# Kernel tuning notes

Measured on AMD Instinct MI355X. Metric: run time of the kernel, lower is better.

The kernel has to match this reference:

```python
import jax, jax.numpy as jnp
import numpy as np

GROUP_SIZE = 64
IN_F, OUT_F, RANK = 4096, 4096, 32
N_TOKENS = 4096
N_GROUPS = IN_F // GROUP_SIZE


def setup_inputs() -> dict:
    key = jax.random.key(0)
    k = jax.random.split(key, 6)
    x = jax.random.normal(k[0], (N_TOKENS, IN_F), dtype=jnp.float32)
    # signed int4 values in [-8, 7], stored unpacked as int32
    main_qweight = jax.random.randint(k[1], (OUT_F, N_GROUPS, GROUP_SIZE), -8, 8, dtype=jnp.int32)
    main_wscale = jax.random.uniform(k[2], (OUT_F, N_GROUPS), dtype=jnp.float32) * 0.02 + 1e-3
    bias = jax.random.normal(k[3], (OUT_F,), dtype=jnp.float32) * 0.02
    proj_down_dense = jax.random.normal(k[4], (IN_F, RANK), dtype=jnp.float32) * 0.02
    proj_up_dense = jax.random.normal(k[5], (RANK, OUT_F), dtype=jnp.float32) * 0.02
    return {
        "x": x,
        "main_qweight": main_qweight,
        "main_wscale": main_wscale,
        "bias": bias,
        "proj_down_dense": proj_down_dense,
        "proj_up_dense": proj_up_dense,
    }


def reference(x, main_qweight, main_wscale, bias, proj_down_dense, proj_up_dense):
    n = x.shape[0]
    # --- per-group int8 activation quantization (symmetric, max-abs/127) ---
    xg = x.reshape(n, N_GROUPS, GROUP_SIZE).astype(jnp.float32)  # [N, G, gs]
    max_abs = jnp.max(jnp.abs(xg), axis=-1, keepdims=True)
    ascale = jnp.where(max_abs > 0, max_abs * (1.0 / 127.0), jnp.ones_like(max_abs))
    qx = jnp.clip(jnp.round(xg / ascale), -127.0, 127.0)
    # Fold per-group activation scales back in; per (out, group) weight scales into weight.
    # out[n,o] = sum_g ascale[n,g] * wscale[o,g] * sum_k qx[n,g,k] * qw[o,g,k]
    a_deq = (qx * ascale).reshape(n, IN_F)                                   # [N, in]
    w_deq = (main_qweight.astype(jnp.float32) * main_wscale[..., None]).reshape(OUT_F, IN_F)  # [out, in]
    out = a_deq @ w_deq.T + bias.astype(jnp.float32)                          # [N, out], fp32 accumulate
    # --- SVD low-rank correction: x @ proj_down @ proj_up (down in x dtype, up in fp32) ---
    low_rank = x @ proj_down_dense                                            # [N, rank]
    out = out + low_rank.astype(jnp.float32) @ proj_up_dense.astype(jnp.float32)
    return out.astype(x.dtype)
```

## Files before the change

kernel.cpp:

```cpp
#include <hip/hip_runtime.h>
#include <hip/hip_bf16.h>

#define IN_F  4096
#define OUT_F 4096
#define NTOK  4096
#define RANK  32
#define GS    64
#define NG    64
#define KTOT  4224
#define NKT   66
#define ITERS 33
#define KCH   1024

typedef __attribute__((ext_vector_type(4))) float f32x4;
typedef __attribute__((ext_vector_type(8))) short bf16x8;

__device__ __forceinline__ ushort f2bf(float f) {
  union { float f; uint u; } c; c.f = f;
  const uint u = c.u;
  return (ushort)((u + 0x7fffu + ((u >> 16) & 1u)) >> 16);
}

__global__ __launch_bounds__(256)
void quant_kernel(const float* __restrict__ x, ushort* __restrict__ Aext)
{
  const int tid  = threadIdx.x;
  const int wave = tid >> 6, lane = tid & 63;
  const int sub  = lane & 15;
  const int ggrp = blockIdx.x * 16 + wave * 4 + (lane >> 4);
  const int row  = ggrp >> 6, g = ggrp & 63;

  const float4 v = *(const float4*)(x + (size_t)row * IN_F + g * GS + sub * 4);
  float m = fmaxf(fmaxf(fabsf(v.x), fabsf(v.y)), fmaxf(fabsf(v.z), fabsf(v.w)));
  m = fmaxf(m, __shfl_xor(m, 1));
  m = fmaxf(m, __shfl_xor(m, 2));
  m = fmaxf(m, __shfl_xor(m, 4));
  m = fmaxf(m, __shfl_xor(m, 8));
  const float ascale = (m > 0.f) ? m * (1.f / 127.f) : 1.f;

  const float d0 = fminf(fmaxf(rintf(v.x / ascale), -127.f), 127.f) * ascale;
  const float d1 = fminf(fmaxf(rintf(v.y / ascale), -127.f), 127.f) * ascale;
  const float d2 = fminf(fmaxf(rintf(v.z / ascale), -127.f), 127.f) * ascale;
  const float d3 = fminf(fmaxf(rintf(v.w / ascale), -127.f), 127.f) * ascale;

  uint2 st;
  st.x = (uint)f2bf(d0) | ((uint)f2bf(d1) << 16);
  st.y = (uint)f2bf(d2) | ((uint)f2bf(d3) << 16);
  *(uint2*)(Aext + (size_t)row * KTOT + g * GS + sub * 4) = st;
}

__global__ __launch_bounds__(256)
void wdeq_kernel(const int* __restrict__ qw, const float* __restrict__ wsc,
                 ushort* __restrict__ Bext)
{
  const int gidx = blockIdx.x * 256 + threadIdx.x;
  const int o  = gidx >> 9;
  const int i0 = (gidx & 511) << 3;
  const float sc = wsc[o * NG + (i0 >> 6)];
  const int4 qa = *(const int4*)(qw + (size_t)o * IN_F + i0);
  const int4 qb = *(const int4*)(qw + (size_t)o * IN_F + i0 + 4);
  uint4 st;
  st.x = (uint)f2bf(qa.x * sc) | ((uint)f2bf(qa.y * sc) << 16);
  st.y = (uint)f2bf(qa.z * sc) | ((uint)f2bf(qa.w * sc) << 16);
  st.z = (uint)f2bf(qb.x * sc) | ((uint)f2bf(qb.y * sc) << 16);
  st.w = (uint)f2bf(qb.z * sc) | ((uint)f2bf(qb.w * sc) << 16);
  *(uint4*)(Bext + (size_t)o * KTOT + i0) = st;
}

__global__ __launch_bounds__(256)
void aux_kernel(const float* __restrict__ pd, const float* __restrict__ pu,
                ushort* __restrict__ Bext, ushort* __restrict__ pdT)
{
  const int id = blockIdx.x * 256 + threadIdx.x;
  ushort* dst = Bext + (size_t)id * KTOT + IN_F;
  #pragma unroll
  for (int r = 0; r < RANK; ++r) {
    dst[r]            = f2bf(pu[(size_t)r * OUT_F + id]);
    dst[RANK + r]     = 0;
    dst[2 * RANK + r] = 0;
    dst[3 * RANK + r] = 0;
  }
  #pragma unroll
  for (int r = 0; r < RANK; ++r)
    pdT[(size_t)r * IN_F + id] = f2bf(pd[(size_t)id * RANK + r]);
}

__global__ __launch_bounds__(256)
void lr_kernel(const ushort* __restrict__ A, const ushort* __restrict__ pdT,
               float* __restrict__ part)
{
  __shared__ alignas(16) ushort lA[64 * 64];
  const int tid  = threadIdx.x;
  const int wave = tid >> 6, lane = tid & 63;
  const int mt = blockIdx.x >> 2;
  const int kc = blockIdx.x & 3;
  const int k0 = kc * KCH;

  const int tr  = tid >> 3;
  const int scc = (tid & 7) ^ (tr & 7);
  const ushort* aSrc = A + (size_t)(mt * 64 + tr) * KTOT + k0 + scc * 8;
  char* ldsA = (char*)lA + wave * 1024;

  f32x4 acc[2];
  #pragma unroll
  for (int n = 0; n < 2; ++n) acc[n] = f32x4{0.f, 0.f, 0.f, 0.f};

  for (int kt = 0; kt < KCH / 64; ++kt) {
    const ushort* aS = aSrc + kt * 64;
    #pragma unroll
    for (int j = 0; j < 2; ++j)
      __builtin_amdgcn_global_load_lds(
          (const __attribute__((address_space(1))) void*)(aS + (size_t)j * 32 * KTOT),
          (__attribute__((address_space(3))) void*)(ldsA + j * 4096), 16, 0, 0);
    __syncthreads();
    #pragma unroll
    for (int ks = 0; ks < 2; ++ks) {
      const int kb  = (ks * 32 + (lane >> 4) * 8) * 2;
      const int row = wave * 16 + (lane & 15);
      const int addr = (row * 128 + kb) ^ ((row & 7) << 4);
      bf16x8 af = *(const bf16x8*)((const char*)lA + addr);
      #pragma unroll
      for (int n = 0; n < 2; ++n) {
        const int prow = n * 16 + (lane & 15);
        bf16x8 bf = *(const bf16x8*)(pdT + (size_t)prow * IN_F + k0 + kt * 64 + ks * 32 + (lane >> 4) * 8);
        acc[n] = __builtin_amdgcn_mfma_f32_16x16x32_bf16(af, bf, acc[n], 0, 0, 0);
      }
    }
    __syncthreads();
  }
  const int r0   = lane & 15;
  const int rowb = mt * 64 + wave * 16 + (lane >> 4) * 4;
  #pragma unroll
  for (int n = 0; n < 2; ++n)
    #pragma unroll
    for (int i = 0; i < 4; ++i)
      part[((size_t)kc * 4096 + rowb + i) * 32 + n * 16 + r0] = acc[n][i];
}

__global__ __launch_bounds__(256)
void lrcomb_kernel(const float* __restrict__ part, ushort* __restrict__ Aext)
{
  const int id  = blockIdx.x * 256 + threadIdx.x;
  const int row = id >> 5, r = id & 31;
  const float s = part[(size_t)row * 32 + r]
                + part[(size_t)(4096 + row) * 32 + r]
                + part[(size_t)(8192 + row) * 32 + r]
                + part[(size_t)(12288 + row) * 32 + r];
  ushort* dst = Aext + (size_t)row * KTOT + IN_F;
  dst[r]            = f2bf(s);
  dst[RANK + r]     = 0;
  dst[2 * RANK + r] = 0;
  dst[3 * RANK + r] = 0;
}

__device__ __forceinline__ void stageA(const ushort* __restrict__ Atile, char* lds,
                                       int b, int h, int kt, int w, int lane)
{
  #pragma unroll
  for (int l = 0; l < 2; ++l) {
    const int g = w * 2 + l;
    const int quarter = h + (g >> 3) * 2;
    const int sub = g & 7;
    const int grow = quarter * 64 + sub * 8 + (lane >> 3);
    const ushort* src = Atile + (size_t)grow * KTOT + kt * 64 + (((lane & 7) ^ (lane >> 3)) << 3);
    __builtin_amdgcn_global_load_lds(
        (const __attribute__((address_space(1))) void*)src,
        (__attribute__((address_space(3))) void*)(lds + b * 32768 + quarter * 8192 + sub * 1024),
        16, 0, 0);
  }
}

__device__ __forceinline__ void stageB(const ushort* __restrict__ Btile, char* lds,
                                       int b, int h, int kt, int w, int lane)
{
  #pragma unroll
  for (int l = 0; l < 2; ++l) {
    const int g = w * 2 + l;
    const int j = g >> 2;
    const int sub = g & 3;
    const int grow = j * 64 + h * 32 + sub * 8 + (lane >> 3);
    const ushort* src = Btile + (size_t)grow * KTOT + kt * 64 + (((lane & 7) ^ (lane >> 3)) << 3);
    __builtin_amdgcn_global_load_lds(
        (const __attribute__((address_space(1))) void*)src,
        (__attribute__((address_space(3))) void*)(lds + 65536 + b * 32768 + j * 8192 + h * 4096 + sub * 1024),
        16, 0, 0);
  }
}

#define PHASE(B_, MQ_, NQ_, STAGE, WAIT4)                                        \
  {                                                                              \
    bf16x8 af[4][2], bfm[2][2];                                                  \
    const int aqb = (B_) * 32768 + (wm * 2 + (MQ_)) * 8192;                      \
    const int bqb = 65536 + (B_) * 32768 + wn * 8192;                            \
    _Pragma("unroll")                                                            \
    for (int mf = 0; mf < 4; ++mf) {                                             \
      const int r = mf * 16 + l15;                                               \
      _Pragma("unroll")                                                          \
      for (int ks = 0; ks < 2; ++ks)                                             \
        af[mf][ks] = *(const bf16x8*)(lds + aqb + (((r * 128) + kbyte[ks]) ^ ((r & 7) << 4))); \
    }                                                                            \
    _Pragma("unroll")                                                            \
    for (int nf = 0; nf < 2; ++nf) {                                             \
      const int r = ((NQ_) * 2 + nf) * 16 + l15;                                 \
      _Pragma("unroll")                                                          \
      for (int ks = 0; ks < 2; ++ks)                                             \
        bfm[nf][ks] = *(const bf16x8*)(lds + bqb + (((r * 128) + kbyte[ks]) ^ ((r & 7) << 4))); \
    }                                                                            \
    STAGE;                                                                       \
    __builtin_amdgcn_s_barrier();                                                \
    __builtin_amdgcn_s_setprio(1);                                               \
    _Pragma("unroll")                                                            \
    for (int mf = 0; mf < 4; ++mf)                                               \
      _Pragma("unroll")                                                          \
      for (int nf = 0; nf < 2; ++nf)                                             \
        _Pragma("unroll")                                                        \
        for (int ks = 0; ks < 2; ++ks)                                           \
          acc[(MQ_) * 4 + mf][(NQ_) * 2 + nf] =                                  \
              __builtin_amdgcn_mfma_f32_16x16x32_bf16(af[mf][ks], bfm[nf][ks],   \
                  acc[(MQ_) * 4 + mf][(NQ_) * 2 + nf], 0, 0, 0);                 \
    __builtin_amdgcn_s_setprio(0);                                               \
    if (WAIT4) asm volatile("s_waitcnt vmcnt(4)" ::: "memory");                  \
    __builtin_amdgcn_s_barrier();                                                \
  }

__global__ __launch_bounds__(512, 2)
void gemm256_kernel(const ushort* __restrict__ A, const ushort* __restrict__ B,
                    const float* __restrict__ bias, float* __restrict__ C)
{
  extern __shared__ char lds[];
  const int tid = threadIdx.x;
  const int w = tid >> 6, lane = tid & 63;
  const int l15 = lane & 15;
  const int wm = w >> 2, wn = w & 3;
  int kbyte[2];
  kbyte[0] = ((lane >> 4) * 8) * 2;
  kbyte[1] = (32 + (lane >> 4) * 8) * 2;

  const int xcd = blockIdx.x & 7, idx = blockIdx.x >> 3;
  const int bm = (xcd >> 1) * 4 + (idx >> 3);
  const int bn = (xcd & 1) * 8 + (idx & 7);

  const ushort* Atile = A + (size_t)bm * 256 * KTOT;
  const ushort* Btile = B + (size_t)bn * 256 * KTOT;

  f32x4 acc[8][4];
  #pragma unroll
  for (int m = 0; m < 8; ++m)
    #pragma unroll
    for (int n = 0; n < 4; ++n)
      acc[m][n] = f32x4{0.f, 0.f, 0.f, 0.f};

  stageA(Atile, lds, 0, 0, 0, w, lane);
  stageB(Btile, lds, 0, 0, 0, w, lane);
  stageB(Btile, lds, 0, 1, 0, w, lane);
  stageA(Atile, lds, 0, 1, 0, w, lane);
  stageA(Atile, lds, 1, 0, 1, w, lane);
  stageB(Btile, lds, 1, 0, 1, w, lane);
  asm volatile("s_waitcnt vmcnt(4)" ::: "memory");
  __builtin_amdgcn_s_barrier();

  #pragma unroll 1
  for (int j = 0; j < ITERS; ++j) {
    const int t1 = 2 * j + 1, t2 = 2 * j + 2, t3 = 2 * j + 3;
    PHASE(0, 0, 0, { stageB(Btile, lds, 1, 1, t1, w, lane); }, 0)
    PHASE(0, 0, 1, { stageA(Atile, lds, 1, 1, t1, w, lane); }, 0)
    PHASE(0, 1, 0, { if (t2 < NKT) stageA(Atile, lds, 0, 0, t2, w, lane); }, 0)
    PHASE(0, 1, 1, { if (t2 < NKT) stageB(Btile, lds, 0, 0, t2, w, lane); }, 1)
    PHASE(1, 0, 0, { if (t2 < NKT) stageB(Btile, lds, 0, 1, t2, w, lane); }, 0)
    PHASE(1, 0, 1, { if (t2 < NKT) stageA(Atile, lds, 0, 1, t2, w, lane); }, 0)
    PHASE(1, 1, 0, { if (t3 < NKT) stageA(Atile, lds, 1, 0, t3, w, lane); }, 0)
    PHASE(1, 1, 1, { if (t3 < NKT) stageB(Btile, lds, 1, 0, t3, w, lane); }, 1)
  }

  const int csub = lane >> 4;
  #pragma unroll
  for (int nf = 0; nf < 4; ++nf) {
    const int col = bn * 256 + wn * 64 + nf * 16 + l15;
    const float bv = bias[col];
    #pragma unroll
    for (int mf = 0; mf < 8; ++mf) {
      const int row = bm * 256 + wm * 128 + mf * 16 + csub * 4;
      #pragma unroll
      for (int i = 0; i < 4; ++i)
        C[(size_t)(row + i) * OUT_F + col] = acc[mf][nf][i] + bv;
    }
  }
}

extern "C" void kernel_launch(void* const* d_in, const int* in_sizes, int n_in,
                              void* d_out, int out_size, void* d_ws, size_t ws_size,
                              hipStream_t stream) {
  const float* x    = (const float*)d_in[0];
  const int*   qw   = (const int*)d_in[1];
  const float* wsc  = (const float*)d_in[2];
  const float* bias = (const float*)d_in[3];
  const float* pd   = (const float*)d_in[4];
  const float* pu   = (const float*)d_in[5];
  float* out = (float*)d_out;

  ushort* Aext = (ushort*)d_ws;
  ushort* Bext = Aext + (size_t)NTOK * KTOT;
  ushort* pdT  = Bext + (size_t)OUT_F * KTOT;
  float*  part = (float*)(pdT + (size_t)RANK * IN_F);

  hipFuncSetAttribute(reinterpret_cast<const void*>(gemm256_kernel),
                      hipFuncAttributeMaxDynamicSharedMemorySize, 131072);

  quant_kernel <<<16384, 256, 0, stream>>>(x, Aext);
  wdeq_kernel  <<< 8192, 256, 0, stream>>>(qw, wsc, Bext);
  aux_kernel   <<<   16, 256, 0, stream>>>(pd, pu, Bext, pdT);
  lr_kernel    <<<  256, 256, 0, stream>>>(Aext, pdT, part);
  lrcomb_kernel<<<  512, 256, 0, stream>>>(part, Aext);
  gemm256_kernel<<< 256, 512, 131072, stream>>>(Aext, Bext, bias, out);
}
```

Before: 202.2 us.

## Switch main GEMM to int8 MFMA with per-group scale epilogue

Keeps activations and weights as int8 with separate per-group scale arrays instead of dequantizing to bf16, and runs the main GEMM with int8 MFMA over 64-wide K groups, applying activation and weight scales in fp32 after each group. The low-rank term is computed straight from x in bf16, then quantized to int8 with a per-row scale and appended as an extra K group. This halves GEMM operand bytes and LDS footprint and uses the higher-rate int8 path. In exchange it adds per-group int-to-float conversion and scaled accumulation, and the extra quantization of the low-rank term and of proj_up is a lossy approximation that may affect accuracy.

Result: slower. 227.0 us (+12.3%).

```diff
diff --git a/kernel.cpp b/kernel.cpp
--- a/kernel.cpp
+++ b/kernel.cpp
@@ -14,15 +14,20 @@
 
 typedef __attribute__((ext_vector_type(4))) float f32x4;
 typedef __attribute__((ext_vector_type(8))) short bf16x8;
+typedef __attribute__((ext_vector_type(4))) int   i32x4;
 
 __device__ __forceinline__ ushort f2bf(float f) {
   union { float f; uint u; } c; c.f = f;
   const uint u = c.u;
   return (ushort)((u + 0x7fffu + ((u >> 16) & 1u)) >> 16);
 }
-
-__global__ __launch_bounds__(256)
-void quant_kernel(const float* __restrict__ x, ushort* __restrict__ Aext)
+__device__ __forceinline__ uint pack4(int a, int b, int c, int d) {
+  return (uint)(a & 255) | ((uint)(b & 255) << 8) | ((uint)(c & 255) << 16) | ((uint)(d & 255) << 24);
+}
+
+__global__ __launch_bounds__(256)
+void quant_kernel(const float* __restrict__ x, char* __restrict__ Aq,
+                  float* __restrict__ AsclT)
 {
   const int tid  = threadIdx.x;
   const int wave = tid >> 6, lane = tid & 63;
@@ -36,58 +41,48 @@
   m = fmaxf(m, __shfl_xor(m, 2));
   m = fmaxf(m, __shfl_xor(m, 4));
   m = fmaxf(m, __shfl_xor(m, 8));
-  const float ascale = (m > 0.f) ? m * (1.f / 127.f) : 1.f;
-
-  const float d0 = fminf(fmaxf(rintf(v.x / ascale), -127.f), 127.f) * ascale;
-  const float d1 = fminf(fmaxf(rintf(v.y / ascale), -127.f), 127.f) * ascale;
-  const float d2 = fminf(fmaxf(rintf(v.z / ascale), -127.f), 127.f) * ascale;
-  const float d3 = fminf(fmaxf(rintf(v.w / ascale), -127.f), 127.f) * ascale;
-
-  uint2 st;
-  st.x = (uint)f2bf(d0) | ((uint)f2bf(d1) << 16);
-  st.y = (uint)f2bf(d2) | ((uint)f2bf(d3) << 16);
-  *(uint2*)(Aext + (size_t)row * KTOT + g * GS + sub * 4) = st;
-}
-
-__global__ __launch_bounds__(256)
-void wdeq_kernel(const int* __restrict__ qw, const float* __restrict__ wsc,
-                 ushort* __restrict__ Bext)
-{
-  const int gidx = blockIdx.x * 256 + threadIdx.x;
-  const int o  = gidx >> 9;
-  const int i0 = (gidx & 511) << 3;
-  const float sc = wsc[o * NG + (i0 >> 6)];
-  const int4 qa = *(const int4*)(qw + (size_t)o * IN_F + i0);
-  const int4 qb = *(const int4*)(qw + (size_t)o * IN_F + i0 + 4);
+  const float as  = (m > 0.f) ? m * (1.f / 127.f) : 1.f;
+  const float inv = (m > 0.f) ? 127.f / m : 1.f;
+
+  const int q0 = (int)fminf(fmaxf(rintf(v.x * inv), -127.f), 127.f);
+  const int q1 = (int)fminf(fmaxf(rintf(v.y * inv), -127.f), 127.f);
+  const int q2 = (int)fminf(fmaxf(rintf(v.z * inv), -127.f), 127.f);
+  const int q3 = (int)fminf(fmaxf(rintf(v.w * inv), -127.f), 127.f);
+
+  *(uint*)(Aq + (size_t)row * KTOT + g * GS + sub * 4) = pack4(q0, q1, q2, q3);
+  if (sub == 0) AsclT[(size_t)g * NTOK + row] = as;
+}
+
+__global__ __launch_bounds__(256)
+void wpack_kernel(const int* __restrict__ qw, const float* __restrict__ wsc,
+                  char* __restrict__ Bq, float* __restrict__ BsclT)
+{
+  const int o = blockIdx.x, t = threadIdx.x;
+  const int4 a = *(const int4*)(qw + (size_t)o * IN_F + t * 16);
+  const int4 b = *(const int4*)(qw + (size_t)o * IN_F + t * 16 + 4);
+  const int4 c = *(const int4*)(qw + (size_t)o * IN_F + t * 16 + 8);
+  const int4 d = *(const int4*)(qw + (size_t)o * IN_F + t * 16 + 12);
   uint4 st;
-  st.x = (uint)f2bf(qa.x * sc) | ((uint)f2bf(qa.y * sc) << 16);
-  st.y = (uint)f2bf(qa.z * sc) | ((uint)f2bf(qa.w * sc) << 16);
-  st.z = (uint)f2bf(qb.x * sc) | ((uint)f2bf(qb.y * sc) << 16);
-  st.w = (uint)f2bf(qb.z * sc) | ((uint)f2bf(qb.w * sc) << 16);
-  *(uint4*)(Bext + (size_t)o * KTOT + i0) = st;
-}
-
-__global__ __launch_bounds__(256)
-void aux_kernel(const float* __restrict__ pd, const float* __restrict__ pu,
-                ushort* __restrict__ Bext, ushort* __restrict__ pdT)
+  st.x = pack4(a.x, a.y, a.z, a.w);
+  st.y = pack4(b.x, b.y, b.z, b.w);
+  st.z = pack4(c.x, c.y, c.z, c.w);
+  st.w = pack4(d.x, d.y, d.z, d.w);
+  *(uint4*)(Bq + (size_t)o * KTOT + t * 16) = st;
+  if (t < NG) BsclT[(size_t)t * OUT_F + o] = wsc[o * NG + t];
+}
+
+__global__ __launch_bounds__(256)
+void pdt_kernel(const float* __restrict__ pd, ushort* __restrict__ pdT)
 {
   const int id = blockIdx.x * 256 + threadIdx.x;
-  ushort* dst = Bext + (size_t)id * KTOT + IN_F;
-  #pragma unroll
-  for (int r = 0; r < RANK; ++r) {
-    dst[r]            = f2bf(pu[(size_t)r * OUT_F + id]);
-    dst[RANK + r]     = 0;
-    dst[2 * RANK + r] = 0;
-    dst[3 * RANK + r] = 0;
-  }
   #pragma unroll
   for (int r = 0; r < RANK; ++r)
     pdT[(size_t)r * IN_F + id] = f2bf(pd[(size_t)id * RANK + r]);
 }
 
 __global__ __launch_bounds__(256)
-void lr_kernel(const ushort* __restrict__ A, const ushort* __restrict__ pdT,
-               float* __restrict__ part)
+void lrx_kernel(const float* __restrict__ x, const ushort* __restrict__ pdT,
+                float* __restrict__ part)
 {
   __shared__ alignas(16) ushort lA[64 * 64];
   const int tid  = threadIdx.x;
@@ -96,22 +91,23 @@
   const int kc = blockIdx.x & 3;
   const int k0 = kc * KCH;
 
-  const int tr  = tid >> 3;
-  const int scc = (tid & 7) ^ (tr & 7);
-  const ushort* aSrc = A + (size_t)(mt * 64 + tr) * KTOT + k0 + scc * 8;
-  char* ldsA = (char*)lA + wave * 1024;
-
   f32x4 acc[2];
   #pragma unroll
   for (int n = 0; n < 2; ++n) acc[n] = f32x4{0.f, 0.f, 0.f, 0.f};
 
   for (int kt = 0; kt < KCH / 64; ++kt) {
-    const ushort* aS = aSrc + kt * 64;
-    #pragma unroll
-    for (int j = 0; j < 2; ++j)
-      __builtin_amdgcn_global_load_lds(
-          (const __attribute__((address_space(1))) void*)(aS + (size_t)j * 32 * KTOT),
-          (__attribute__((address_space(3))) void*)(ldsA + j * 4096), 16, 0, 0);
+    __syncthreads();
+    #pragma unroll
+    for (int s = 0; s < 4; ++s) {
+      const int row = (tid >> 4) + s * 16;
+      const int c4  = tid & 15;
+      const float4 v = *(const float4*)(x + (size_t)(mt * 64 + row) * IN_F + k0 + kt * 64 + c4 * 4);
+      uint2 p;
+      p.x = (uint)f2bf(v.x) | ((uint)f2bf(v.y) << 16);
+      p.y = (uint)f2bf(v.z) | ((uint)f2bf(v.w) << 16);
+      const int addr = (row * 128 + c4 * 8) ^ ((row & 7) << 4);
+      *(uint2*)((char*)lA + addr) = p;
+    }
     __syncthreads();
     #pragma unroll
     for (int ks = 0; ks < 2; ++ks) {
@@ -126,7 +122,6 @@
         acc[n] = __builtin_amdgcn_mfma_f32_16x16x32_bf16(af, bf, acc[n], 0, 0, 0);
       }
     }
-    __syncthreads();
   }
   const int r0   = lane & 15;
   const int rowb = mt * 64 + wave * 16 + (lane >> 4) * 4;
@@ -138,7 +133,8 @@
 }
 
 __global__ __launch_bounds__(256)
-void lrcomb_kernel(const float* __restrict__ part, ushort* __restrict__ Aext)
+void lrq_kernel(const float* __restrict__ part, char* __restrict__ Aq,
+                float* __restrict__ AsclT)
 {
   const int id  = blockIdx.x * 256 + threadIdx.x;
   const int row = id >> 5, r = id & 31;
@@ -146,102 +142,167 @@
                 + part[(size_t)(4096 + row) * 32 + r]
                 + part[(size_t)(8192 + row) * 32 + r]
                 + part[(size_t)(12288 + row) * 32 + r];
-  ushort* dst = Aext + (size_t)row * KTOT + IN_F;
-  dst[r]            = f2bf(s);
-  dst[RANK + r]     = 0;
-  dst[2 * RANK + r] = 0;
-  dst[3 * RANK + r] = 0;
-}
-
-__device__ __forceinline__ void stageA(const ushort* __restrict__ Atile, char* lds,
-                                       int b, int h, int kt, int w, int lane)
-{
-  #pragma unroll
-  for (int l = 0; l < 2; ++l) {
-    const int g = w * 2 + l;
-    const int quarter = h + (g >> 3) * 2;
-    const int sub = g & 7;
-    const int grow = quarter * 64 + sub * 8 + (lane >> 3);
-    const ushort* src = Atile + (size_t)grow * KTOT + kt * 64 + (((lane & 7) ^ (lane >> 3)) << 3);
-    __builtin_amdgcn_global_load_lds(
-        (const __attribute__((address_space(1))) void*)src,
-        (__attribute__((address_space(3))) void*)(lds + b * 32768 + quarter * 8192 + sub * 1024),
-        16, 0, 0);
-  }
-}
-
-__device__ __forceinline__ void stageB(const ushort* __restrict__ Btile, char* lds,
-                                       int b, int h, int kt, int w, int lane)
-{
-  #pragma unroll
-  for (int l = 0; l < 2; ++l) {
-    const int g = w * 2 + l;
-    const int j = g >> 2;
-    const int sub = g & 3;
-    const int grow = j * 64 + h * 32 + sub * 8 + (lane >> 3);
-    const ushort* src = Btile + (size_t)grow * KTOT + kt * 64 + (((lane & 7) ^ (lane >> 3)) << 3);
-    __builtin_amdgcn_global_load_lds(
-        (const __attribute__((address_space(1))) void*)src,
-        (__attribute__((address_space(3))) void*)(lds + 65536 + b * 32768 + j * 8192 + h * 4096 + sub * 1024),
-        16, 0, 0);
-  }
-}
-
-#define PHASE(B_, MQ_, NQ_, STAGE, WAIT4)                                        \
+  float m = fabsf(s);
+  m = fmaxf(m, __shfl_xor(m, 1));
+  m = fmaxf(m, __shfl_xor(m, 2));
+  m = fmaxf(m, __shfl_xor(m, 4));
+  m = fmaxf(m, __shfl_xor(m, 8));
+  m = fmaxf(m, __shfl_xor(m, 16));
+  const float as  = (m > 0.f) ? m * (1.f / 127.f) : 1.f;
+  const float inv = (m > 0.f) ? 127.f / m : 1.f;
+  const int q = (int)fminf(fmaxf(rintf(s * inv), -127.f), 127.f);
+  char* dst = Aq + (size_t)row * KTOT + IN_F;
+  dst[r]        = (char)q;
+  dst[RANK + r] = 0;
+  if (r == 0) {
+    AsclT[(size_t)64 * NTOK + row] = as;
+    AsclT[(size_t)65 * NTOK + row] = 0.f;
+  }
+}
+
+__global__ __launch_bounds__(256)
+void puq_kernel(const float* __restrict__ pu, char* __restrict__ Bq,
+                float* __restrict__ BsclT)
+{
+  const int o = blockIdx.x * 256 + threadIdx.x;
+  float v[RANK]; float m = 0.f;
+  #pragma unroll
+  for (int r = 0; r < RANK; ++r) {
+    v[r] = pu[(size_t)r * OUT_F + o];
+    m = fmaxf(m, fabsf(v[r]));
+  }
+  const float ws  = (m > 0.f) ? m * (1.f / 127.f) : 1.f;
+  const float inv = (m > 0.f) ? 127.f / m : 1.f;
+  uint b[8];
+  #pragma unroll
+  for (int u = 0; u < 8; ++u) {
+    int q[4];
+    #pragma unroll
+    for (int k = 0; k < 4; ++k)
+      q[k] = (int)fminf(fmaxf(rintf(v[u * 4 + k] * inv), -127.f), 127.f);
+    b[u] = pack4(q[0], q[1], q[2], q[3]);
+  }
+  char* dst = Bq + (size_t)o * KTOT + IN_F;
+  *(uint4*)(dst)      = uint4{b[0], b[1], b[2], b[3]};
+  *(uint4*)(dst + 16) = uint4{b[4], b[5], b[6], b[7]};
+  *(uint4*)(dst + 32) = uint4{0, 0, 0, 0};
+  *(uint4*)(dst + 48) = uint4{0, 0, 0, 0};
+  BsclT[(size_t)64 * OUT_F + o] = ws;
+  BsclT[(size_t)65 * OUT_F + o] = 0.f;
+}
+
+__device__ __forceinline__ void stageA_i8(const char* __restrict__ Atile, char* lds,
+                                          int b, int h, int t, int w, int lane)
+{
+  const int quarter = h + ((w >> 2) << 1);
+  const int rq      = ((w & 3) << 4) + (lane >> 2);
+  const int schunk  = (lane & 3) ^ ((rq >> 1) & 3);
+  const char* src = Atile + (size_t)(quarter * 64 + rq) * KTOT + t * 64 + schunk * 16;
+  __builtin_amdgcn_global_load_lds(
+      (const __attribute__((address_space(1))) void*)src,
+      (__attribute__((address_space(3))) void*)(lds + b * 16384 + quarter * 4096 + ((w & 3) << 10)),
+      16, 0, 0);
+}
+
+__device__ __forceinline__ void stageB_i8(const char* __restrict__ Btile, char* lds,
+                                          int b, int h, int t, int w, int lane)
+{
+  const int j  = w >> 1;
+  const int rr = (h << 5) + ((w & 1) << 4) + (lane >> 2);
+  const int schunk = (lane & 3) ^ ((rr >> 1) & 3);
+  const char* src = Btile + (size_t)(j * 64 + rr) * KTOT + t * 64 + schunk * 16;
+  __builtin_amdgcn_global_load_lds(
+      (const __attribute__((address_space(1))) void*)src,
+      (__attribute__((address_space(3))) void*)(lds + 32768 + b * 16384 + j * 4096 + (h << 11) + ((w & 1) << 10)),
+      16, 0, 0);
+}
+
+__device__ __forceinline__ void stageSclA(const float* __restrict__ AsclT, char* lds,
+                                          int b, int t, int bm, int lane)
+{
+  const float* src = AsclT + (size_t)t * NTOK + bm * 256 + lane * 4;
+  __builtin_amdgcn_global_load_lds(
+      (const __attribute__((address_space(1))) void*)src,
+      (__attribute__((address_space(3))) void*)(lds + 65536 + b * 1024), 16, 0, 0);
+}
+
+__device__ __forceinline__ void stageSclB(const float* __restrict__ BsclT, char* lds,
+                                          int b, int t, int bn, int lane)
+{
+  const float* src = BsclT + (size_t)t * OUT_F + bn * 256 + lane * 4;
+  __builtin_amdgcn_global_load_lds(
+      (const __attribute__((address_space(1))) void*)src,
+      (__attribute__((address_space(3))) void*)(lds + 67584 + b * 1024), 16, 0, 0);
+}
+
+#define PHASE(B_, MQ_, NQ_, STAGE, WAIT2)                                        \
   {                                                                              \
-    bf16x8 af[4][2], bfm[2][2];                                                  \
-    const int aqb = (B_) * 32768 + (wm * 2 + (MQ_)) * 8192;                      \
-    const int bqb = 65536 + (B_) * 32768 + wn * 8192;                            \
+    const int aq = wm * 2 + (MQ_);                                               \
+    i32x4 af[4], bfm[2];                                                         \
+    f32x4 as4[4];                                                                \
+    float wsv[2];                                                                \
     _Pragma("unroll")                                                            \
     for (int mf = 0; mf < 4; ++mf) {                                             \
       const int r = mf * 16 + l15;                                               \
-      _Pragma("unroll")                                                          \
-      for (int ks = 0; ks < 2; ++ks)                                             \
-        af[mf][ks] = *(const bf16x8*)(lds + aqb + (((r * 128) + kbyte[ks]) ^ ((r & 7) << 4))); \
+      af[mf] = *(const i32x4*)(lds + (B_) * 16384 + aq * 4096 +                  \
+                               ((r * 64 + k16 * 16) ^ (((r >> 1) & 3) << 4)));   \
     }                                                                            \
     _Pragma("unroll")                                                            \
     for (int nf = 0; nf < 2; ++nf) {                                             \
-      const int r = ((NQ_) * 2 + nf) * 16 + l15;                                 \
-      _Pragma("unroll")                                                          \
-      for (int ks = 0; ks < 2; ++ks)                                             \
-        bfm[nf][ks] = *(const bf16x8*)(lds + bqb + (((r * 128) + kbyte[ks]) ^ ((r & 7) << 4))); \
+      const int r = (NQ_) * 32 + nf * 16 + l15;                                  \
+      bfm[nf] = *(const i32x4*)(lds + 32768 + (B_) * 16384 + wn * 4096 +         \
+                                ((r * 64 + k16 * 16) ^ (((r >> 1) & 3) << 4)));  \
     }                                                                            \
+    _Pragma("unroll")                                                            \
+    for (int mf = 0; mf < 4; ++mf)                                               \
+      as4[mf] = *(const f32x4*)(lds + 65536 + (B_) * 1024 +                      \
+                                aq * 256 + mf * 64 + (lane >> 4) * 16);          \
+    _Pragma("unroll")                                                            \
+    for (int nf = 0; nf < 2; ++nf)                                               \
+      wsv[nf] = *(const float*)(lds + 67584 + (B_) * 1024 +                      \
+                                (wn * 64 + (NQ_) * 32 + nf * 16 + l15) * 4);     \
     STAGE;                                                                       \
     __builtin_amdgcn_s_barrier();                                                \
     __builtin_amdgcn_s_setprio(1);                                               \
+    i32x4 d8[4][2];                                                              \
     _Pragma("unroll")                                                            \
     for (int mf = 0; mf < 4; ++mf)                                               \
       _Pragma("unroll")                                                          \
       for (int nf = 0; nf < 2; ++nf)                                             \
-        _Pragma("unroll")                                                        \
-        for (int ks = 0; ks < 2; ++ks)                                           \
-          acc[(MQ_) * 4 + mf][(NQ_) * 2 + nf] =                                  \
-              __builtin_amdgcn_mfma_f32_16x16x32_bf16(af[mf][ks], bfm[nf][ks],   \
-                  acc[(MQ_) * 4 + mf][(NQ_) * 2 + nf], 0, 0, 0);                 \
+        d8[mf][nf] = __builtin_amdgcn_mfma_i32_16x16x64_i8(                      \
+            af[mf], bfm[nf], (i32x4){0, 0, 0, 0}, 0, 0, 0);                      \
+    _Pragma("unroll")                                                            \
+    for (int mf = 0; mf < 4; ++mf)                                               \
+      _Pragma("unroll")                                                          \
+      for (int nf = 0; nf < 2; ++nf) {                                           \
+        f32x4 df;                                                                \
+        df[0] = (float)d8[mf][nf][0]; df[1] = (float)d8[mf][nf][1];              \
+        df[2] = (float)d8[mf][nf][2]; df[3] = (float)d8[mf][nf][3];              \
+        acc[(MQ_) * 4 + mf][(NQ_) * 2 + nf] += as4[mf] * (wsv[nf] * df);         \
+      }                                                                          \
     __builtin_amdgcn_s_setprio(0);                                               \
-    if (WAIT4) asm volatile("s_waitcnt vmcnt(4)" ::: "memory");                  \
+    if (WAIT2) asm volatile("s_waitcnt vmcnt(2)" ::: "memory");                  \
     __builtin_amdgcn_s_barrier();                                                \
   }
 
 __global__ __launch_bounds__(512, 2)
-void gemm256_kernel(const ushort* __restrict__ A, const ushort* __restrict__ B,
+void gemm256_kernel(const char* __restrict__ A, const char* __restrict__ B,
+                    const float* __restrict__ AsclT, const float* __restrict__ BsclT,
                     const float* __restrict__ bias, float* __restrict__ C)
 {
   extern __shared__ char lds[];
   const int tid = threadIdx.x;
   const int w = tid >> 6, lane = tid & 63;
   const int l15 = lane & 15;
+  const int k16 = lane >> 4;
   const int wm = w >> 2, wn = w & 3;
-  int kbyte[2];
-  kbyte[0] = ((lane >> 4) * 8) * 2;
-  kbyte[1] = (32 + (lane >> 4) * 8) * 2;
 
   const int xcd = blockIdx.x & 7, idx = blockIdx.x >> 3;
   const int bm = (xcd >> 1) * 4 + (idx >> 3);
   const int bn = (xcd & 1) * 8 + (idx & 7);
 
-  const ushort* Atile = A + (size_t)bm * 256 * KTOT;
-  const ushort* Btile = B + (size_t)bn * 256 * KTOT;
+  const char* Atile = A + (size_t)bm * 256 * KTOT;
+  const char* Btile = B + (size_t)bn * 256 * KTOT;
 
   f32x4 acc[8][4];
   #pragma unroll
@@ -250,26 +311,34 @@
     for (int n = 0; n < 4; ++n)
       acc[m][n] = f32x4{0.f, 0.f, 0.f, 0.f};
 
-  stageA(Atile, lds, 0, 0, 0, w, lane);
-  stageB(Btile, lds, 0, 0, 0, w, lane);
-  stageB(Btile, lds, 0, 1, 0, w, lane);
-  stageA(Atile, lds, 0, 1, 0, w, lane);
-  stageA(Atile, lds, 1, 0, 1, w, lane);
-  stageB(Btile, lds, 1, 0, 1, w, lane);
-  asm volatile("s_waitcnt vmcnt(4)" ::: "memory");
+  stageA_i8(Atile, lds, 0, 0, 0, w, lane);
+  stageB_i8(Btile, lds, 0, 0, 0, w, lane);
+  stageSclA(AsclT, lds, 0, 0, bm, lane);
+  stageSclB(BsclT, lds, 0, 0, bn, lane);
+  stageA_i8(Atile, lds, 0, 1, 0, w, lane);
+  stageB_i8(Btile, lds, 0, 1, 0, w, lane);
+  stageA_i8(Atile, lds, 1, 0, 1, w, lane);
+  stageB_i8(Btile, lds, 1, 0, 1, w, lane);
+  asm volatile("s_waitcnt vmcnt(2)" ::: "memory");
   __builtin_amdgcn_s_barrier();
 
   #pragma unroll 1
   for (int j = 0; j < ITERS; ++j) {
-    const int t1 = 2 * j + 1, t2 = 2 * j + 2, t3 = 2 * j + 3;
-    PHASE(0, 0, 0, { stageB(Btile, lds, 1, 1, t1, w, lane); }, 0)
-    PHASE(0, 0, 1, { stageA(Atile, lds, 1, 1, t1, w, lane); }, 0)
-    PHASE(0, 1, 0, { if (t2 < NKT) stageA(Atile, lds, 0, 0, t2, w, lane); }, 0)
-    PHASE(0, 1, 1, { if (t2 < NKT) stageB(Btile, lds, 0, 0, t2, w, lane); }, 1)
-    PHASE(1, 0, 0, { if (t2 < NKT) stageB(Btile, lds, 0, 1, t2, w, lane); }, 0)
-    PHASE(1, 0, 1, { if (t2 < NKT) stageA(Atile, lds, 0, 1, t2, w, lane); }, 0)
-    PHASE(1, 1, 0, { if (t3 < NKT) stageA(Atile, lds, 1, 0, t3, w, lane); }, 0)
-    PHASE(1, 1, 1, { if (t3 < NKT) stageB(Btile, lds, 1, 0, t3, w, lane); }, 1)
+    const int t1 = 2 * j + 1;
+    const int t2 = (2 * j + 2 < NKT) ? 2 * j + 2 : NKT - 1;
+    const int t3 = (2 * j + 3 < NKT) ? 2 * j + 3 : NKT - 1;
+    PHASE(0, 0, 0, { stageB_i8(Btile, lds, 1, 1, t1, w, lane);
+                     stageSclA(AsclT, lds, 1, t1, bm, lane); }, 0)
+    PHASE(0, 0, 1, { stageA_i8(Atile, lds, 1, 1, t1, w, lane);
+                     stageSclB(BsclT, lds, 1, t1, bn, lane); }, 0)
+    PHASE(0, 1, 0, { stageA_i8(Atile, lds, 0, 0, t2, w, lane); }, 0)
+    PHASE(0, 1, 1, { stageB_i8(Btile, lds, 0, 0, t2, w, lane); }, 1)
+    PHASE(1, 0, 0, { stageB_i8(Btile, lds, 0, 1, t2, w, lane);
+                     stageSclA(AsclT, lds, 0, t2, bm, lane); }, 0)
+    PHASE(1, 0, 1, { stageA_i8(Atile, lds, 0, 1, t2, w, lane);
+                     stageSclB(BsclT, lds, 0, t2, bn, lane); }, 0)
+    PHASE(1, 1, 0, { stageA_i8(Atile, lds, 1, 0, t3, w, lane); }, 0)
+    PHASE(1, 1, 1, { stageB_i8(Btile, lds, 1, 0, t3, w, lane); }, 1)
   }
 
   const int csub = lane >> 4;
@@ -298,18 +367,21 @@
   const float* pu   = (const float*)d_in[5];
   float* out = (float*)d_out;
 
-  ushort* Aext = (ushort*)d_ws;
-  ushort* Bext = Aext + (size_t)NTOK * KTOT;
-  ushort* pdT  = Bext + (size_t)OUT_F * KTOT;
-  float*  part = (float*)(pdT + (size_t)RANK * IN_F);
+  char*  Aq    = (char*)d_ws;
+  char*  Bq    = Aq + (size_t)NTOK * KTOT;
+  float* AsclT = (float*)(Bq + (size_t)OUT_F * KTOT);
+  float* BsclT = AsclT + (size_t)NKT * NTOK;
+  ushort* pdT  = (ushort*)(BsclT + (size_t)NKT * OUT_F);
+  float* part  = (float*)(pdT + (size_t)RANK * IN_F);
 
   hipFuncSetAttribute(reinterpret_cast<const void*>(gemm256_kernel),
-                      hipFuncAttributeMaxDynamicSharedMemorySize, 131072);
-
-  quant_kernel <<<16384, 256, 0, stream>>>(x, Aext);
-  wdeq_kernel  <<< 8192, 256, 0, stream>>>(qw, wsc, Bext);
-  aux_kernel   <<<   16, 256, 0, stream>>>(pd, pu, Bext, pdT);
-  lr_kernel    <<<  256, 256, 0, stream>>>(Aext, pdT, part);
-  lrcomb_kernel<<<  512, 256, 0, stream>>>(part, Aext);
-  gemm256_kernel<<< 256, 512, 131072, stream>>>(Aext, Bext, bias, out);
-}
+                      hipFuncAttributeMaxDynamicSharedMemorySize, 69632);
+
+  quant_kernel<<<16384, 256, 0, stream>>>(x, Aq, AsclT);
+  wpack_kernel<<< 4096, 256, 0, stream>>>(qw, wsc, Bq, BsclT);
+  pdt_kernel  <<<   16, 256, 0, stream>>>(pd, pdT);
+  lrx_kernel  <<<  256, 256, 0, stream>>>(x, pdT, part);
+  lrq_kernel  <<<  512, 256, 0, stream>>>(part, Aq, AsclT);
+  puq_kernel  <<<   16, 256, 0, stream>>>(pu, Bq, BsclT);
+  gemm256_kernel<<<256, 512, 69632, stream>>>(Aq, Bq, AsclT, BsclT, bias, out);
+}
```

## Reuse LDS fragments across phases with register double-buffering in GEMM main loop

Applied to the files above, without the earlier changes.

Restructures the 8-phase main loop so A and B fragments are kept in registers (X/Y double buffers) and reused across quadrant MFMA blocks instead of reloaded every phase. It cuts LDS reads per k-tile, overlaps fragment reads with MFMA, and issues the next tile's reads before the loop back. In the last iteration the tile indices are clamped to a valid tile instead of skipping the stage, which adds redundant loads. It also adds more barriers and more live registers, which under launch_bounds(512,2) risks spills.

After: 372.7 us. 1.84x slower.

```diff
diff --git a/kernel.cpp b/kernel.cpp
--- a/kernel.cpp
+++ b/kernel.cpp
@@ -187,41 +187,47 @@
   }
 }
 
-#define PHASE(B_, MQ_, NQ_, STAGE, WAIT4)                                        \
+#define READ_AF(DST, B_, MQ_)                                                    \
   {                                                                              \
-    bf16x8 af[4][2], bfm[2][2];                                                  \
     const int aqb = (B_) * 32768 + (wm * 2 + (MQ_)) * 8192;                      \
-    const int bqb = 65536 + (B_) * 32768 + wn * 8192;                            \
     _Pragma("unroll")                                                            \
     for (int mf = 0; mf < 4; ++mf) {                                             \
       const int r = mf * 16 + l15;                                               \
       _Pragma("unroll")                                                          \
       for (int ks = 0; ks < 2; ++ks)                                             \
-        af[mf][ks] = *(const bf16x8*)(lds + aqb + (((r * 128) + kbyte[ks]) ^ ((r & 7) << 4))); \
+        DST[mf][ks] = *(const bf16x8*)(lds + aqb +                               \
+            (((r * 128) + kbyte[ks]) ^ ((r & 7) << 4)));                         \
     }                                                                            \
+  }
+
+#define READ_BF(DST, B_, NQ_)                                                    \
+  {                                                                              \
+    const int bqb = 65536 + (B_) * 32768 + wn * 8192;                            \
     _Pragma("unroll")                                                            \
     for (int nf = 0; nf < 2; ++nf) {                                             \
       const int r = ((NQ_) * 2 + nf) * 16 + l15;                                 \
       _Pragma("unroll")                                                          \
       for (int ks = 0; ks < 2; ++ks)                                             \
-        bfm[nf][ks] = *(const bf16x8*)(lds + bqb + (((r * 128) + kbyte[ks]) ^ ((r & 7) << 4))); \
+        DST[nf][ks] = *(const bf16x8*)(lds + bqb +                               \
+            (((r * 128) + kbyte[ks]) ^ ((r & 7) << 4)));                         \
     }                                                                            \
-    STAGE;                                                                       \
-    __builtin_amdgcn_s_barrier();                                                \
-    __builtin_amdgcn_s_setprio(1);                                               \
+  }
+
+#define MFMA16(MQ_, NQ_, AF, BF)                                                 \
+  __builtin_amdgcn_s_setprio(1);                                                 \
+  _Pragma("unroll")                                                              \
+  for (int mf = 0; mf < 4; ++mf)                                                 \
     _Pragma("unroll")                                                            \
-    for (int mf = 0; mf < 4; ++mf)                                               \
+    for (int nf = 0; nf < 2; ++nf)                                               \
       _Pragma("unroll")                                                          \
-      for (int nf = 0; nf < 2; ++nf)                                             \
-        _Pragma("unroll")                                                        \
-        for (int ks = 0; ks < 2; ++ks)                                           \
-          acc[(MQ_) * 4 + mf][(NQ_) * 2 + nf] =                                  \
-              __builtin_amdgcn_mfma_f32_16x16x32_bf16(af[mf][ks], bfm[nf][ks],   \
-                  acc[(MQ_) * 4 + mf][(NQ_) * 2 + nf], 0, 0, 0);                 \
-    __builtin_amdgcn_s_setprio(0);                                               \
-    if (WAIT4) asm volatile("s_waitcnt vmcnt(4)" ::: "memory");                  \
-    __builtin_amdgcn_s_barrier();                                                \
-  }
+      for (int ks = 0; ks < 2; ++ks)                                             \
+        acc[(MQ_) * 4 + mf][(NQ_) * 2 + nf] =                                    \
+            __builtin_amdgcn_mfma_f32_16x16x32_bf16(AF[mf][ks], BF[nf][ks],      \
+                acc[(MQ_) * 4 + mf][(NQ_) * 2 + nf], 0, 0, 0);                   \
+  __builtin_amdgcn_s_setprio(0);
+
+#define BAR __builtin_amdgcn_s_barrier()
+#define DRAIN4 asm volatile("s_waitcnt vmcnt(4)" ::: "memory")
 
 __global__ __launch_bounds__(512, 2)
 void gemm256_kernel(const ushort* __restrict__ A, const ushort* __restrict__ B,
@@ -250,26 +256,67 @@
     for (int n = 0; n < 4; ++n)
       acc[m][n] = f32x4{0.f, 0.f, 0.f, 0.f};
 
+  bf16x8 afX[4][2], afY[4][2], b0X[2][2], b0Y[2][2], b1[2][2];
+
   stageA(Atile, lds, 0, 0, 0, w, lane);
   stageB(Btile, lds, 0, 0, 0, w, lane);
   stageB(Btile, lds, 0, 1, 0, w, lane);
   stageA(Atile, lds, 0, 1, 0, w, lane);
   stageA(Atile, lds, 1, 0, 1, w, lane);
   stageB(Btile, lds, 1, 0, 1, w, lane);
-  asm volatile("s_waitcnt vmcnt(4)" ::: "memory");
-  __builtin_amdgcn_s_barrier();
+  DRAIN4;
+  BAR;
+  READ_AF(afX, 0, 0);
+  READ_BF(b0X, 0, 0);
 
   #pragma unroll 1
   for (int j = 0; j < ITERS; ++j) {
-    const int t1 = 2 * j + 1, t2 = 2 * j + 2, t3 = 2 * j + 3;
-    PHASE(0, 0, 0, { stageB(Btile, lds, 1, 1, t1, w, lane); }, 0)
-    PHASE(0, 0, 1, { stageA(Atile, lds, 1, 1, t1, w, lane); }, 0)
-    PHASE(0, 1, 0, { if (t2 < NKT) stageA(Atile, lds, 0, 0, t2, w, lane); }, 0)
-    PHASE(0, 1, 1, { if (t2 < NKT) stageB(Btile, lds, 0, 0, t2, w, lane); }, 1)
-    PHASE(1, 0, 0, { if (t2 < NKT) stageB(Btile, lds, 0, 1, t2, w, lane); }, 0)
-    PHASE(1, 0, 1, { if (t2 < NKT) stageA(Atile, lds, 0, 1, t2, w, lane); }, 0)
-    PHASE(1, 1, 0, { if (t3 < NKT) stageA(Atile, lds, 1, 0, t3, w, lane); }, 0)
-    PHASE(1, 1, 1, { if (t3 < NKT) stageB(Btile, lds, 1, 0, t3, w, lane); }, 1)
+    const int t1 = 2 * j + 1;
+    const int t2 = (2 * j + 2 < NKT) ? 2 * j + 2 : NKT - 1;
+    const int t3 = (2 * j + 3 < NKT) ? 2 * j + 3 : NKT - 1;
+
+    stageB(Btile, lds, 1, 1, t1, w, lane);
+    BAR;
+    READ_BF(b1, 0, 1);
+    MFMA16(0, 0, afX, b0X);
+    BAR;
+    stageA(Atile, lds, 1, 1, t1, w, lane);
+    BAR;
+    READ_AF(afY, 0, 1);
+    MFMA16(0, 1, afX, b1);
+    BAR;
+    stageA(Atile, lds, 0, 0, t2, w, lane);
+    BAR;
+    MFMA16(1, 1, afY, b1);
+    BAR;
+    stageB(Btile, lds, 0, 0, t2, w, lane);
+    DRAIN4;
+    BAR;
+    READ_AF(afX, 1, 0);
+    READ_BF(b0Y, 1, 0);
+    MFMA16(1, 0, afY, b0X);
+    BAR;
+    stageB(Btile, lds, 0, 1, t2, w, lane);
+    BAR;
+    READ_BF(b1, 1, 1);
+    MFMA16(0, 0, afX, b0Y);
+    BAR;
+    stageA(Atile, lds, 0, 1, t2, w, lane);
+    BAR;
+    READ_AF(afY, 1, 1);
+    MFMA16(0, 1, afX, b1);
+    BAR;
+    stageA(Atile, lds, 1, 0, t3, w, lane);
+    BAR;
+    MFMA16(1, 1, afY, b1);
+    BAR;
+    stageB(Btile, lds, 1, 0, t3, w, lane);
+    DRAIN4;
+    BAR;
+    READ_AF(afX, 0, 0);
+    READ_BF(b0X, 0, 0);
+    MFMA16(1, 0, afY, b0Y);
+    BAR;
   }
 
   const int csub = lane >> 4;
```
